# Performance work log

Measured on AMD Instinct MI355X. Metric: run time of the kernel, lower is better.

Reference implementation:

```python
import jax, jax.numpy as jnp
import numpy as np

H, KV, D = 12, 4, 128  # n_head, n_kv_head, head_dim
VE_GATE_CH = 12

def _rmsnorm(x):
    eps = jnp.finfo(x.dtype).eps  # matches torch F.rms_norm default eps
    return x * jax.lax.rsqrt(jnp.mean(x * x, axis=-1, keepdims=True) + eps)

def _rope(x, cos, sin):
    d = x.shape[-1] // 2
    x1, x2 = x[..., :d], x[..., d:]
    return jnp.concatenate([x1 * cos + x2 * sin, -x1 * sin + x2 * cos], axis=-1)

def setup_inputs() -> dict:
    key = jax.random.key(0)
    ks = jax.random.split(key, 9)
    B, T, C = 2, 2048, 1536
    x = jax.random.normal(ks[0], (B, T, C), jnp.float32)
    ve = jax.random.normal(ks[1], (B, T, KV * D), jnp.float32)
    ang = jax.random.uniform(ks[2], (1, T, 1, D // 2), jnp.float32) * (2.0 * np.pi)
    cos, sin = jnp.cos(ang), jnp.sin(ang)
    Wq = jax.random.normal(ks[3], (H * D, C), jnp.float32) * 0.02
    Wk = jax.random.normal(ks[4], (KV * D, C), jnp.float32) * 0.02
    Wv = jax.random.normal(ks[5], (KV * D, C), jnp.float32) * 0.02
    Wproj = jax.random.normal(ks[6], (C, C), jnp.float32) * 0.02
    Wg = jax.random.normal(ks[7], (KV, VE_GATE_CH), jnp.float32) * 0.02
    return dict(x=x, ve=ve, cos=cos, sin=sin, Wq=Wq, Wk=Wk, Wv=Wv, Wproj=Wproj, Wg=Wg, window=1024)

def reference(x, ve, cos, sin, Wq, Wk, Wv, Wproj, Wg, window):
    B, T, C = x.shape
    q = (x @ Wq.T).reshape(B, T, H, D)
    k = (x @ Wk.T).reshape(B, T, KV, D)
    v = (x @ Wv.T).reshape(B, T, KV, D)
    # value-embedding gate: 3*sigmoid(Linear(x[..., :12])) per kv head
    gate = 3.0 * jax.nn.sigmoid(x[..., :VE_GATE_CH] @ Wg.T)  # [B,T,KV]
    v = v + gate[..., None] * ve.reshape(B, T, KV, D)
    q = _rmsnorm(_rope(q, cos, sin)) * 1.2
    k = _rmsnorm(_rope(k, cos, sin)) * 1.2
    rep = H // KV  # GQA group size
    qh = q.transpose(0, 2, 1, 3).reshape(B, KV, rep, T, D)
    kh = k.transpose(0, 2, 1, 3)  # [B,KV,T,D]
    vh = v.transpose(0, 2, 1, 3)
    scores = jnp.einsum('bgrtd,bgsd->bgrts', qh, kh) / np.sqrt(D)
    row = jnp.arange(T)[:, None]
    col = jnp.arange(T)[None, :]
    if window < 0 or window >= T:
        mask = col <= row  # pure causal
    else:
        mask = (col <= row) & (row - col <= window)  # causal sliding window
    scores = jnp.where(mask, scores, -jnp.inf)
    att = jax.nn.softmax(scores, axis=-1)
    y = jnp.einsum('bgrts,bgsd->bgrtd', att, vh)
    y = y.reshape(B, H, T, D).transpose(0, 2, 1, 3).reshape(B, T, H * D)
    return y @ Wproj.T
```

## Files before the change

kernel.cpp:

```cpp
#include <hip/hip_runtime.h>
#include <hip/hip_bf16.h>
#include <math.h>

#define B_  2
#define T_  2048
#define C_  1536
#define H_  12
#define KV_ 4
#define D_  128
#define M_  (B_*T_)
#define REP_ (H_/KV_)
#define NQKV_ 2560
#define KK_  1536
#define NKT_ 24

typedef __bf16 bf16x8 __attribute__((ext_vector_type(8)));
typedef float  f32x4  __attribute__((ext_vector_type(4)));
typedef unsigned u32x4 __attribute__((ext_vector_type(4)));

union BCast { u32x4 u; bf16x8 b; };

__device__ inline bf16x8 ldb8(const ushort* p) {
    BCast c; c.u = *reinterpret_cast<const u32x4*>(p); return c.b;
}

__device__ inline ushort f2bf(float f) {
    union { float f; unsigned u; } v; v.f = f;
    unsigned u = v.u;
    return (ushort)((u + 0x7FFF + ((u >> 16) & 1)) >> 16);
}

__device__ inline float bf2f(ushort u) {
    union { unsigned u; float f; } v; v.u = (unsigned)u << 16;
    return v.f;
}

__device__ inline void async_copy16(const ushort* g, ushort* l) {
    __builtin_amdgcn_global_load_lds(
        (const __attribute__((address_space(1))) unsigned*)g,
        (__attribute__((address_space(3))) unsigned*)l, 16, 0, 0);
}

__device__ __host__ inline int dperm(int d) {
    return (d < 32) ? d : (d < 64 ? d + 32 : (d < 96 ? d - 32 : d));
}

__device__ __forceinline__ void lgkm0_fence() {
    __builtin_amdgcn_s_waitcnt(0xC07F);
    __builtin_amdgcn_sched_barrier(0);
}

#define MFMA16(va, vb, d) d = __builtin_amdgcn_mfma_f32_16x16x32_bf16(va, vb, d, 0, 0, 0)

#define CLUSTER(AARR, BARR, MB, NB)                                        \
    __builtin_amdgcn_s_setprio(1);                                         \
    _Pragma("unroll")                                                      \
    for (int mf = 0; mf < 4; mf++)                                         \
        _Pragma("unroll")                                                  \
        for (int nf = 0; nf < 2; nf++) {                                   \
            MFMA16(AARR[mf*2+0], BARR[nf*2+0], acc[(MB)+mf][(NB)+nf]);     \
            MFMA16(AARR[mf*2+1], BARR[nf*2+1], acc[(MB)+mf][(NB)+nf]);     \
        }                                                                  \
    __builtin_amdgcn_s_setprio(0);

#define RD_AL(bo_) { _Pragma("unroll") for (int mf = 0; mf < 4; mf++) {    \
        aL[mf*2+0] = ldb8(aB0 + (bo_) + mf*1024);                          \
        aL[mf*2+1] = ldb8(aB1 + (bo_) + mf*1024); } }
#define RD_AH(bo_) { _Pragma("unroll") for (int mf = 0; mf < 4; mf++) {    \
        aH[mf*2+0] = ldb8(aB0 + (bo_) + 4096 + mf*1024);                   \
        aH[mf*2+1] = ldb8(aB1 + (bo_) + 4096 + mf*1024); } }
#define RD_B0(bo_) { _Pragma("unroll") for (int nf = 0; nf < 2; nf++) {    \
        b0[nf*2+0] = ldb8(bB0 + (bo_) + nf*1024);                          \
        b0[nf*2+1] = ldb8(bB1 + (bo_) + nf*1024); } }
#define RD_B1(bo_) { _Pragma("unroll") for (int nf = 0; nf < 2; nf++) {    \
        b1[nf*2+0] = ldb8(bB0 + (bo_) + 2048 + nf*1024);                   \
        b1[nf*2+1] = ldb8(bB1 + (bo_) + 2048 + nf*1024); } }

template<int EPI>
__global__ __launch_bounds__(512) void gemm256(const ushort* __restrict__ A,
                                               const ushort* __restrict__ Bm,
                                               ushort* __restrict__ Qp,
                                               ushort* __restrict__ Kp,
                                               ushort* __restrict__ vbuf,
                                               float* __restrict__ Cf,
                                               const float* __restrict__ cosb,
                                               const float* __restrict__ sinb) {
    __shared__ ushort lds[2][2][2][8192];
    const int tid  = threadIdx.x;
    const int wave = tid >> 6, lane = tid & 63;
    const int m16 = lane & 15, quad = lane >> 4;
    const int WM = wave >> 2, WN = wave & 3;
    const int brow = (WN & 1) << 6;

    const int nwg  = gridDim.x * gridDim.y;
    const int orig = blockIdx.y * gridDim.x + blockIdx.x;
    const int vid  = (orig & 7) * (nwg >> 3) + (orig >> 3);
    const int bxT  = vid >> 4;
    const int byT  = vid & 15;
    const int bm = byT << 8, bn = bxT << 8;

    const int r = tid >> 3;
    const int slot8 = ((tid & 7) ^ (r & 7)) << 3;
    const ushort* Ag = A  + (size_t)(bm + r) * KK_ + slot8;
    const ushort* Bg = Bm + (size_t)(bn + r) * KK_ + slot8;
    const size_t row64 = (size_t)64 * KK_;
    const size_t hskip = (size_t)128 * KK_;

    auto stage2 = [&](const ushort* Gp, int buf, int op, int kc) {
        ushort* base = &lds[0][0][0][0] + op * 32768 + buf * 16384 + wave * 512;
        const ushort* g = Gp + kc;
        async_copy16(g,                 base);
        async_copy16(g + row64,         base + 4096);
        async_copy16(g + hskip,         base + 8192);
        async_copy16(g + hskip + row64, base + 8192 + 4096);
    };

    const int swzu = (m16 & 7) << 3;
    const int k0u  = (quad * 8) ^ swzu;
    const int k1u  = (32 + quad * 8) ^ swzu;
    const ushort* ldsu = &lds[0][0][0][0];
    const ushort* aB0 = ldsu + (WM ? 8192 : 0) + (m16 << 6) + k0u;
    const ushort* aB1 = ldsu + (WM ? 8192 : 0) + (m16 << 6) + k1u;
    const ushort* bB0 = ldsu + 32768 + ((WN >> 1) ? 8192 : 0) + ((brow + m16) << 6) + k0u;
    const ushort* bB1 = ldsu + 32768 + ((WN >> 1) ? 8192 : 0) + ((brow + m16) << 6) + k1u;

    f32x4 acc[8][4];
    #pragma unroll
    for (int i = 0; i < 8; i++)
        #pragma unroll
        for (int j = 0; j < 4; j++) acc[i][j] = (f32x4){0.f, 0.f, 0.f, 0.f};

    bf16x8 aL[8], aH[8], b0[4], b1[4];

    stage2(Bg, 0, 1, 0);  stage2(Ag, 0, 0, 0);
    stage2(Bg, 1, 1, 64); stage2(Ag, 1, 0, 64);
    __builtin_amdgcn_s_waitcnt(0x0F78);
    __builtin_amdgcn_sched_barrier(0);
    __builtin_amdgcn_s_barrier();
    __builtin_amdgcn_sched_barrier(0);
    RD_AL(0); RD_B0(0);

    #pragma unroll 1
    for (int kt = 0; kt < NKT_ - 1; kt++) {
        const int bo  = (kt & 1) ? 16384 : 0;
        const int boN = 16384 - bo;
        const bool stg = (kt < NKT_ - 2);
        const int kc2 = (kt + 2) << 6;
        lgkm0_fence();
        RD_B1(bo);
        CLUSTER(aL, b0, 0, 0);
        lgkm0_fence();
        RD_AH(bo);
        CLUSTER(aL, b1, 0, 2);
        lgkm0_fence();
        __builtin_amdgcn_s_barrier();
        __builtin_amdgcn_sched_barrier(0);
        if (stg) {
            stage2(Bg, kt & 1, 1, kc2);
            stage2(Ag, kt & 1, 0, kc2);
            __builtin_amdgcn_s_waitcnt(0x0F78);
        } else {
            __builtin_amdgcn_s_waitcnt(0x0F70);
        }
        __builtin_amdgcn_sched_barrier(0);
        __builtin_amdgcn_s_barrier();
        __builtin_amdgcn_sched_barrier(0);
        CLUSTER(aH, b0, 4, 0);
        RD_AL(boN); RD_B0(boN);
        CLUSTER(aH, b1, 4, 2);
    }
    {
        const int bo = ((NKT_ - 1) & 1) ? 16384 : 0;
        lgkm0_fence();
        RD_B1(bo);
        CLUSTER(aL, b0, 0, 0);
        lgkm0_fence();
        RD_AH(bo);
        CLUSTER(aL, b1, 0, 2);
        lgkm0_fence();
        CLUSTER(aH, b0, 4, 0);
        CLUSTER(aH, b1, 4, 2);
    }
    __syncthreads();

    if constexpr (EPI == 0) {
        if (bn >= 2048) {
            const int cb = bn - 2048 + WN*64;
            #pragma unroll
            for (int m = 0; m < 8; m++) {
                const int rl = WM*128 + (m>>2)*64 + (m&3)*16 + quad*4;
                #pragma unroll
                for (int reg = 0; reg < 4; reg++) {
                    ushort* vr = vbuf + (size_t)(bm + rl + reg) * 512 + cb + m16;
                    #pragma unroll
                    for (int j = 0; j < 4; j++)
                        vr[(j>>1)*32 + (j&1)*16] = f2bf(acc[m][j][reg]);
                }
            }
        } else {
            float* ssqS = (float*)&lds[0][0][0][0];
            #pragma unroll
            for (int m = 0; m < 8; m++) {
                #pragma unroll
                for (int reg = 0; reg < 4; reg++) {
                    float v = acc[m][0][reg]*acc[m][0][reg] + acc[m][1][reg]*acc[m][1][reg]
                            + acc[m][2][reg]*acc[m][2][reg] + acc[m][3][reg]*acc[m][3][reg];
                    v += __shfl_xor(v, 1); v += __shfl_xor(v, 2);
                    v += __shfl_xor(v, 4); v += __shfl_xor(v, 8);
                    if (m16 == 0) {
                        const int rl = WM*128 + (m>>2)*64 + (m&3)*16 + quad*4 + reg;
                        ssqS[rl*4 + WN] = v;
                    }
                }
            }
            __syncthreads();

            const bool isq = (bn < 1536);
            const float osc = isq ? (1.2f * 1.2f * 0.08838834764831845f) : 1.0f;
            const int hh = (isq ? (bn >> 7) : ((bn - 1536) >> 7)) + (WN >> 1);
            const int nh  = isq ? H_ : KV_;
            ushort* outp  = isq ? Qp : Kp;

            #pragma unroll
            for (int m = 0; m < 8; m++) {
                #pragma unroll
                for (int reg = 0; reg < 4; reg++) {
                    const int rl = WM*128 + (m>>2)*64 + (m&3)*16 + quad*4 + reg;
                    const int row = bm + rl;
                    const float tot = ssqS[rl*4 + (WN & ~1)] + ssqS[rl*4 + (WN | 1)];
                    const float sc = rsqrtf(tot * (1.0f/128.0f) + 1.1920928955078125e-07f) * osc;
                    const int b = row >> 11, t = row & (T_ - 1);
                    ushort* orow = outp + ((size_t)(b * nh + hh) * T_ + t) * D_;
                    #pragma unroll
                    for (int nf = 0; nf < 2; nf++) {
                        const int ipair = (WN & 1) * 32 + nf*16 + m16;
                        const float c = cosb[t*64 + ipair], s = sinb[t*64 + ipair];
                        const float x1 = acc[m][nf][reg], x2 = acc[m][2+nf][reg];
                        const int oc = (WN & 1) * 64 + nf*16 + m16;
                        orow[oc]      = f2bf((x1*c + x2*s) * sc);
                        orow[oc + 32] = f2bf((x2*c - x1*s) * sc);
                    }
                }
            }
        }
    } else {
        #pragma unroll
        for (int m = 0; m < 8; m++) {
            const int rl = WM*128 + (m>>2)*64 + (m&3)*16 + quad*4;
            #pragma unroll
            for (int reg = 0; reg < 4; reg++) {
                float* cr = Cf + (size_t)(bm + rl + reg) * C_ + bn + WN*64 + m16;
                #pragma unroll
                for (int j = 0; j < 4; j++)
                    cr[(j>>1)*32 + (j&1)*16] = acc[m][j][reg];
            }
        }
    }
}

#define SEG0 1572864
#define SEG1 2162688
#define SEG2 2359296
#define SEG3 2555904
#define SEG4 3145728
#define ROW4 384
__global__ __launch_bounds__(256) void cast_all(const float* __restrict__ x,
                                                const float* __restrict__ Wq,
                                                const float* __restrict__ Wk,
                                                const float* __restrict__ Wv,
                                                const float* __restrict__ Wp,
                                                ushort* __restrict__ xb,
                                                ushort* __restrict__ Wqkvb,
                                                ushort* __restrict__ Wpb) {
    const int i = blockIdx.x * 256 + threadIdx.x;
    float4 v; size_t dst4; ushort* dstp;
    if (i < SEG0) {
        v = ((const float4*)x)[i]; dstp = xb; dst4 = i;
    } else if (i < SEG1) {
        const int j = i - SEG0;
        const int r = j / ROW4, c4 = j - r * ROW4;
        const int d = r & 127, hh = r >> 7;
        v = ((const float4*)Wq)[j]; dstp = Wqkvb;
        dst4 = (size_t)(hh * 128 + dperm(d)) * ROW4 + c4;
    } else if (i < SEG2) {
        const int j = i - SEG1;
        const int r = j / ROW4, c4 = j - r * ROW4;
        const int d = r & 127, g = r >> 7;
        v = ((const float4*)Wk)[j]; dstp = Wqkvb;
        dst4 = (size_t)(1536 + g * 128 + dperm(d)) * ROW4 + c4;
    } else if (i < SEG3) {
        const int j = i - SEG2;
        v = ((const float4*)Wv)[j]; dstp = Wqkvb;
        dst4 = (size_t)2048 * ROW4 + j;
    } else {
        const int j = i - SEG3;
        v = ((const float4*)Wp)[j]; dstp = Wpb; dst4 = j;
    }
    ((ushort4*)dstp)[dst4] = make_ushort4(f2bf(v.x), f2bf(v.y), f2bf(v.z), f2bf(v.w));
}

__global__ __launch_bounds__(256) void gate_vt(const ushort* __restrict__ vbuf,
                                               const float* __restrict__ x,
                                               const float* __restrict__ ve,
                                               const float* __restrict__ Wg,
                                               ushort* __restrict__ Vt) {
    const int t0 = blockIdx.x * 64, g = blockIdx.y, b = blockIdx.z;
    __shared__ float gateS[64];
    __shared__ ushort tile[128][66];
    const int tid = threadIdx.x;
    if (tid < 64) {
        const float* xr = x + (size_t)(b * T_ + t0 + tid) * C_;
        float acc = 0.f;
        #pragma unroll
        for (int c = 0; c < 12; c++) acc += xr[c] * Wg[g * 12 + c];
        gateS[tid] = 3.0f / (1.0f + __expf(-acc));
    }
    __syncthreads();
    #pragma unroll
    for (int i = 0; i < 32; i++) {
        int idx = i * 256 + tid;
        int r = idx >> 7;
        int d = idx & 127;
        size_t offv = (size_t)(b * T_ + t0 + r) * 512 + g * D_ + d;
        tile[d][r] = f2bf(bf2f(vbuf[offv]) + gateS[r] * ve[offv]);
    }
    __syncthreads();
    ushort* ob = Vt + ((size_t)(b * KV_ + g) * D_) * T_ + t0;
    #pragma unroll
    for (int i = 0; i < 32; i++) {
        int idx = i * 256 + tid;
        int d = idx >> 6;
        int c = idx & 63;
        ob[(size_t)d * T_ + c] = tile[d][c];
    }
}

__global__ __launch_bounds__(256, 3) void attn_mfma(const ushort* __restrict__ Qp,
                                                    const ushort* __restrict__ Kp,
                                                    const ushort* __restrict__ Vt,
                                                    ushort* __restrict__ Y,
                                                    const int* __restrict__ wptr) {
    const int t0 = blockIdx.x * 64;
    const int h  = blockIdx.y, b = blockIdx.z;
    const int g  = h / REP_;
    const int tid  = threadIdx.x;
    const int wave = tid >> 6, lane = tid & 63;
    const int m16 = lane & 15, quad = lane >> 4;

    __shared__ ushort Ks[4 * 32 * 32];
    __shared__ ushort Vs[128 * 32];
    __shared__ ushort Pl[4][16 * 40];

    const int w = *wptr;
    const bool windowed = (w >= 0 && w < T_);
    const unsigned wu = windowed ? (unsigned)w : 0x7FFFFFFFu;
    int s_lo = 0;
    if (windowed) { s_lo = t0 - w; if (s_lo < 0) s_lo = 0; }
    const int s_hi = t0 + 63;
    const int ss0 = s_lo & ~31;
    const int tw = t0 + wave * 16;

    const ushort* qrow = Qp + ((size_t)(b * H_ + h) * T_ + tw + m16) * D_ + quad * 8;
    bf16x8 qa[4];
    #pragma unroll
    for (int kc = 0; kc < 4; kc++) qa[kc] = ldb8(qrow + kc * 32);

    const ushort* kbase = Kp + (size_t)(b * KV_ + g) * T_ * D_;
    const ushort* vbase = Vt + (size_t)(b * KV_ + g) * D_ * T_;

    const int c0 = wave, c1 = wave + 4;
    const ushort* kg0 = kbase + (size_t)((c0 & 1) * 16 + (lane >> 2)) * D_ + (c0 >> 1) * 32 + (lane & 3) * 8;
    const ushort* kg1 = kbase + (size_t)((c1 & 1) * 16 + (lane >> 2)) * D_ + (c1 >> 1) * 32 + (lane & 3) * 8;
    ushort* kl0 = Ks + c0 * 512;
    ushort* kl1 = Ks + c1 * 512;
    const ushort* vg0 = vbase + (size_t)(c0 * 16 + (lane >> 2)) * T_ + (lane & 3) * 8;
    const ushort* vg1 = vbase + (size_t)(c1 * 16 + (lane >> 2)) * T_ + (lane & 3) * 8;
    ushort* vl0 = Vs + c0 * 512;
    ushort* vl1 = Vs + c1 * 512;

    f32x4 o[8];
    #pragma unroll
    for (int dt = 0; dt < 8; dt++) o[dt] = (f32x4){0.f, 0.f, 0.f, 0.f};
    f32x4 lacc = (f32x4){0.f, 0.f, 0.f, 0.f};
    BCast onesc; onesc.u = (u32x4){0x3F803F80u, 0x3F803F80u, 0x3F803F80u, 0x3F803F80u};
    const bf16x8 ones = onesc.b;
    ushort* pw = &Pl[wave][0];

    for (int ss = ss0; ss <= s_hi; ss += 32) {
        const size_t koff = (size_t)ss * D_;
        async_copy16(kg0 + koff, kl0);
        async_copy16(kg1 + koff, kl1);
        async_copy16(vg0 + ss,   vl0);
        async_copy16(vg1 + ss,   vl1);
        __syncthreads();

        f32x4 s0 = (f32x4){0.f,0.f,0.f,0.f};
        f32x4 s1 = (f32x4){0.f,0.f,0.f,0.f};
        #pragma unroll
        for (int kc = 0; kc < 4; kc++) {
            bf16x8 kf0 = ldb8(Ks + kc * 1024 + m16 * 32 + quad * 8);
            bf16x8 kf1 = ldb8(Ks + kc * 1024 + (16 + m16) * 32 + quad * 8);
            s0 = __builtin_amdgcn_mfma_f32_16x16x32_bf16(qa[kc], kf0, s0, 0, 0, 0);
            s1 = __builtin_amdgcn_mfma_f32_16x16x32_bf16(qa[kc], kf1, s1, 0, 0, 0);
        }

        const int sA = ss + m16, sB = ss + 16 + m16;
        #pragma unroll
        for (int reg = 0; reg < 4; reg++) {
            const int t = tw + quad * 4 + reg;
            const float pa = ((unsigned)(t - sA) <= wu) ? __expf(s0[reg]) : 0.f;
            const float pb = ((unsigned)(t - sB) <= wu) ? __expf(s1[reg]) : 0.f;
            pw[(quad * 4 + reg) * 40 + m16]      = f2bf(pa);
            pw[(quad * 4 + reg) * 40 + 16 + m16] = f2bf(pb);
        }

        __builtin_amdgcn_s_waitcnt(0xc07f);
        bf16x8 pfrag = ldb8(pw + m16 * 40 + quad * 8);

        #pragma unroll
        for (int dt = 0; dt < 8; dt++) {
            bf16x8 vf = ldb8(Vs + (dt * 16 + m16) * 32 + quad * 8);
            o[dt] = __builtin_amdgcn_mfma_f32_16x16x32_bf16(pfrag, vf, o[dt], 0, 0, 0);
        }
        lacc = __builtin_amdgcn_mfma_f32_16x16x32_bf16(pfrag, ones, lacc, 0, 0, 0);
        __syncthreads();
    }

    float inv[4];
    #pragma unroll
    for (int reg = 0; reg < 4; reg++) inv[reg] = 1.0f / lacc[reg];
    ushort* yb = Y + ((size_t)(b * T_ + tw + quad * 4) * H_ + h) * D_ + m16;
    #pragma unroll
    for (int reg = 0; reg < 4; reg++)
        #pragma unroll
        for (int dt = 0; dt < 8; dt++)
            yb[(size_t)reg * H_ * D_ + dt * 16] = f2bf(o[dt][reg] * inv[reg]);
}

extern "C" void kernel_launch(void* const* d_in, const int* in_sizes, int n_in,
                              void* d_out, int out_size, void* d_ws, size_t ws_size,
                              hipStream_t stream) {
    const float* x     = (const float*)d_in[0];
    const float* ve    = (const float*)d_in[1];
    const float* cosb  = (const float*)d_in[2];
    const float* sinb  = (const float*)d_in[3];
    const float* Wq    = (const float*)d_in[4];
    const float* Wk    = (const float*)d_in[5];
    const float* Wv    = (const float*)d_in[6];
    const float* Wproj = (const float*)d_in[7];
    const float* Wg    = (const float*)d_in[8];
    const int*   wptr  = (const int*)d_in[9];
    float* out = (float*)d_out;

    ushort* xb    = (ushort*)d_ws;
    ushort* vbuf  = xb    + (size_t)M_ * C_;
    ushort* Qp    = vbuf  + (size_t)M_ * 512;
    ushort* Kp    = Qp    + (size_t)M_ * C_;
    ushort* Vt    = Kp    + (size_t)M_ * 512;
    ushort* yb16  = Vt    + (size_t)M_ * 512;
    ushort* Wqkvb = yb16  + (size_t)M_ * C_;
    ushort* Wpb   = Wqkvb + (size_t)NQKV_ * C_;

    cast_all<<<SEG4 / 256, 256, 0, stream>>>(x, Wq, Wk, Wv, Wproj, xb, Wqkvb, Wpb);

    gemm256<0><<<dim3(NQKV_ / 256, M_ / 256), 512, 0, stream>>>(
        xb, Wqkvb, Qp, Kp, vbuf, nullptr, cosb, sinb);

    gate_vt<<<dim3(T_ / 64, KV_, B_), 256, 0, stream>>>(vbuf, x, ve, Wg, Vt);

    attn_mfma<<<dim3(T_ / 64, H_, B_), 256, 0, stream>>>(Qp, Kp, Vt, yb16, wptr);

    gemm256<1><<<dim3(C_ / 256, M_ / 256), 512, 0, stream>>>(
        yb16, Wpb, nullptr, nullptr, nullptr, out, nullptr, nullptr);
}
```

Before: 262.8 us.

## Simplify GEMM main loop: load all fragments per k-tile, drop register prefetch

Reworks the bf16 GEMM K-loop. The old loop software-pipelined LDS-to-register fragment reads across iterations, using explicit lgkmcnt fences. The new loop reads all A and B fragments for the current tile at the top, then runs the four MFMA clusters separated by s_barriers, and keeps the global-to-LDS double-buffer staging. This gives up the overlap between LDS reads and MFMA work across iterations and adds extra workgroup barriers, relying on the compiler to schedule the waits instead.

Result: slower. 269.3 us (+2.5%).

```diff
diff --git a/kernel.cpp b/kernel.cpp
--- a/kernel.cpp
+++ b/kernel.cpp
@@ -43,11 +43,6 @@
 
 __device__ __host__ inline int dperm(int d) {
     return (d < 32) ? d : (d < 64 ? d + 32 : (d < 96 ? d - 32 : d));
-}
-
-__device__ __forceinline__ void lgkm0_fence() {
-    __builtin_amdgcn_s_waitcnt(0xC07F);
-    __builtin_amdgcn_sched_barrier(0);
 }
 
 #define MFMA16(va, vb, d) d = __builtin_amdgcn_mfma_f32_16x16x32_bf16(va, vb, d, 0, 0, 0)
@@ -130,56 +125,40 @@
         #pragma unroll
         for (int j = 0; j < 4; j++) acc[i][j] = (f32x4){0.f, 0.f, 0.f, 0.f};
 
-    bf16x8 aL[8], aH[8], b0[4], b1[4];
-
     stage2(Bg, 0, 1, 0);  stage2(Ag, 0, 0, 0);
     stage2(Bg, 1, 1, 64); stage2(Ag, 1, 0, 64);
     __builtin_amdgcn_s_waitcnt(0x0F78);
     __builtin_amdgcn_sched_barrier(0);
     __builtin_amdgcn_s_barrier();
     __builtin_amdgcn_sched_barrier(0);
-    RD_AL(0); RD_B0(0);
 
     #pragma unroll 1
-    for (int kt = 0; kt < NKT_ - 1; kt++) {
-        const int bo  = (kt & 1) ? 16384 : 0;
-        const int boN = 16384 - bo;
-        const bool stg = (kt < NKT_ - 2);
-        const int kc2 = (kt + 2) << 6;
-        lgkm0_fence();
-        RD_B1(bo);
+    for (int kt = 0; kt < NKT_; kt++) {
+        const int bo = (kt & 1) ? 16384 : 0;
+        bf16x8 aL[8], aH[8], b0[4], b1[4];
+        RD_AL(bo); RD_B0(bo); RD_B1(bo); RD_AH(bo);
         CLUSTER(aL, b0, 0, 0);
-        lgkm0_fence();
-        RD_AH(bo);
+        __builtin_amdgcn_s_barrier();
         CLUSTER(aL, b1, 0, 2);
-        lgkm0_fence();
         __builtin_amdgcn_s_barrier();
-        __builtin_amdgcn_sched_barrier(0);
-        if (stg) {
-            stage2(Bg, kt & 1, 1, kc2);
-            stage2(Ag, kt & 1, 0, kc2);
-            __builtin_amdgcn_s_waitcnt(0x0F78);
-        } else {
-            __builtin_amdgcn_s_waitcnt(0x0F70);
-        }
-        __builtin_amdgcn_sched_barrier(0);
+        CLUSTER(aH, b1, 4, 2);
         __builtin_amdgcn_s_barrier();
-        __builtin_amdgcn_sched_barrier(0);
         CLUSTER(aH, b0, 4, 0);
-        RD_AL(boN); RD_B0(boN);
-        CLUSTER(aH, b1, 4, 2);
-    }
-    {
-        const int bo = ((NKT_ - 1) & 1) ? 16384 : 0;
-        lgkm0_fence();
-        RD_B1(bo);
-        CLUSTER(aL, b0, 0, 0);
-        lgkm0_fence();
-        RD_AH(bo);
-        CLUSTER(aL, b1, 0, 2);
-        lgkm0_fence();
-        CLUSTER(aH, b0, 4, 0);
-        CLUSTER(aH, b1, 4, 2);
+        if (kt < NKT_ - 1) {
+            __builtin_amdgcn_sched_barrier(0);
+            __builtin_amdgcn_s_barrier();
+            __builtin_amdgcn_sched_barrier(0);
+            if (kt < NKT_ - 2) {
+                stage2(Bg, kt & 1, 1, (kt + 2) << 6);
+                stage2(Ag, kt & 1, 0, (kt + 2) << 6);
+                __builtin_amdgcn_s_waitcnt(0x0F78);
+            } else {
+                __builtin_amdgcn_s_waitcnt(0x0F70);
+            }
+            __builtin_amdgcn_sched_barrier(0);
+            __builtin_amdgcn_s_barrier();
+            __builtin_amdgcn_sched_barrier(0);
+        }
     }
     __syncthreads();
 
```
